# Optimization experiments

Measured on AMD Instinct MI355X. Metric: run time of the kernel, lower is better.

## Reference

```python
import jax, jax.numpy as jnp
import numpy as np

N = 100_000      # nodes
E_HALF = 1_600_000  # undirected edges (mirrored -> 3.2M directed)
D = 128          # feature dim
K = 1            # k-MIS hop parameter


def setup_inputs() -> dict:
    key = jax.random.key(0)
    k1, k2, k3, k4, k5 = jax.random.split(key, 5)
    x = jax.random.normal(k1, (N, D), dtype=jnp.float32)
    src = jax.random.randint(k2, (E_HALF,), 0, N)
    dst = jax.random.randint(k3, (E_HALF,), 0, N)
    # symmetric edge list (undirected graph), as k-MIS coverage assumes
    edge_index = jnp.stack([jnp.concatenate([src, dst]),
                            jnp.concatenate([dst, src])])
    ea = jax.random.uniform(k4, (E_HALF,), dtype=jnp.float32)
    edge_attr = jnp.concatenate([ea, ea])
    # RandomScorer: score is a uniform random vector over nodes
    score = jax.random.uniform(k5, (N,), dtype=jnp.float32)
    return {"x": x, "edge_index": edge_index, "edge_attr": edge_attr, "score": score}


def _scatter_min(values, index, n, fill):
    return jnp.full((n,), fill, dtype=values.dtype).at[index].min(values)


def maximal_k_independent_set(row, col, n, k, rank):
    # Iteratively: propagate min rank k hops; nodes equal to their own
    # (uncovered) min rank join the MIS; mark their k-hop neighborhood covered.
    mis = jnp.zeros(n, dtype=bool)
    mask = jnp.zeros(n, dtype=bool)
    min_rank = rank
    while not bool(mask.all()):
        for _ in range(k):
            mn = _scatter_min(min_rank[row], col, n, n)
            min_rank = jnp.minimum(mn, min_rank)
        mis = mis | ((rank == min_rank) & ~mask)
        mask = mask | mis
        for _ in range(k):
            nb = jnp.zeros(n, dtype=bool).at[col].max(mask[row])
            mask = mask | nb
        min_rank = jnp.where(mask, n, rank)
    return mis


def cluster_k_mis(mis, row, col, n, k, rank):
    # assign every node to the MIS node of minimum rank within k hops
    min_rank = jnp.where(mis, rank, n)
    for _ in range(k):
        mn = _scatter_min(min_rank[row], col, n, n)
        min_rank = jnp.minimum(mn, min_rank)
    _, clusters = jnp.unique(min_rank, return_inverse=True)  # sorted uniques
    perm = jnp.argsort(rank[mis])  # sorted-rank position -> index into x[mis]
    return perm[clusters.ravel()]


def reference(x, edge_index, edge_attr, score):
    n = x.shape[0]
    row, col = edge_index[0], edge_index[1]
    # Greedy ordering: rank = inverse permutation of argsort(score)
    rank = jnp.argsort(jnp.argsort(score))
    mis = maximal_k_independent_set(row, col, n, K, rank)
    cluster = cluster_k_mis(mis, row, col, n, K, rank)
    # sparse_reduce_adj: map edges into cluster space, coalesce with sum
    pairs = jnp.stack([cluster[row], cluster[col]], axis=1)  # [E,2]
    uk, inv = jnp.unique(pairs, axis=0, return_inverse=True)
    vals = jax.ops.segment_sum(edge_attr, inv.ravel(), num_segments=uk.shape[0])
    r2, c2 = uk[:, 0], uk[:, 1]
    keep = r2 != c2  # remove_self_loops
    edge_index_out = jnp.stack([r2[keep], c2[keep]])
    edge_attr_out = vals[keep]
    x_out = x[jnp.nonzero(mis)[0]]  # reduce_x=None -> select MIS node features
    return x_out, edge_index_out, edge_attr_out, cluster, mis, score
```

## Files before the change

### kernel.cpp

```cpp
#include <hip/hip_runtime.h>
#include <stdint.h>

#define RTILE 4096
#define ROUNDS 10


__global__ void k_init_counters(int* counters){
  int t = threadIdx.x;
  counters[t] = 0;
  if (t == 7) counters[7] = 1;
}
__global__ void k_init_nodes(int* mis, int N){
  int v = blockIdx.x*blockDim.x + threadIdx.x;
  if (v < N) mis[v]=0;
}
__global__ void k_zero_vals(float* vals, int E){
  int i = blockIdx.x*blockDim.x + threadIdx.x;
  if (i < E) vals[i]=0.f;
}

__global__ void k_score_key(const float* score, unsigned* keys, unsigned* pay, int N){
  int i = blockIdx.x*blockDim.x+threadIdx.x;
  if (i<N){
    unsigned b = __float_as_uint(score[i]);
    b ^= ((int)b < 0) ? 0xFFFFFFFFu : 0x80000000u;
    keys[i]=b; pay[i]=(unsigned)i;
  }
}
__global__ void k_rank_build(const unsigned* pay, int* rank, int* pm, int N){
  int p = blockIdx.x*blockDim.x+threadIdx.x;
  if (p<N){ int v = (int)pay[p]; rank[v]=p; pm[v]=p; }
}
__global__ void k_make_colrow(const int* __restrict__ row, const int* __restrict__ col,
                              unsigned* __restrict__ keys, unsigned* __restrict__ pay, int E){
  int e = blockIdx.x*blockDim.x+threadIdx.x;
  if (e<E){ keys[e]=(unsigned)col[e]; pay[e]=(unsigned)row[e]; }
}

template<typename K, int TILE>
__global__ void k_radix_hist(const K* __restrict__ keys, int n, int shift,
                             unsigned* __restrict__ ghist, int numBlocks, const int* gate){
  if (*gate==0) return;
  __shared__ unsigned h[512];
  int t=threadIdx.x, b=blockIdx.x;
  h[t]=0; h[t+256]=0; __syncthreads();
  int base = b*TILE;
  for (int j=t; j<TILE; j+=256){
    int i = base+j;
    if (i<n){
      unsigned d = (unsigned)((keys[i]>>shift)&(K)511);
      atomicAdd(&h[d],1u);
    }
  }
  __syncthreads();
  ghist[(size_t)t*numBlocks + b] = h[t];
  ghist[(size_t)(t+256)*numBlocks + b] = h[t+256];
}

template<typename K, int TILE>
__global__ __launch_bounds__(256)
void k_radix_scatter(const K* __restrict__ keysIn, const unsigned* __restrict__ payIn,
                     K* __restrict__ keysOut, unsigned* __restrict__ payOut,
                     int n, int shift, const unsigned* __restrict__ gbase,
                     int numBlocks, const int* gate){
  if (*gate==0) return;
  constexpr int G = TILE/256;
  constexpr int SEG = TILE/4;
  __shared__ __align__(16) char smem[(size_t)TILE*sizeof(K)];
  K* skey = (K*)smem;
  unsigned* spay = (unsigned*)smem;
  __shared__ unsigned whist[4][512];
  __shared__ unsigned lbase[512];
  __shared__ unsigned ss[256];
  int t=threadIdx.x, b=blockIdx.x;
  int lane = t&63, wave = t>>6;
  int base = b*TILE;
  int tilecnt = min(TILE, n-base);
  int segBase = base + wave*SEG;

  for (int j=lane; j<512; j+=64) whist[wave][j]=0;
  K keys[G]; unsigned pays[G];
  for (int g=0; g<G; ++g){
    int i = segBase + g*64 + lane;
    bool valid = i<n;
    keys[g] = valid ? keysIn[i] : (K)0;
    pays[g] = valid ? payIn[i] : 0u;
    if (valid){
      unsigned d = (unsigned)((keys[g]>>shift)&(K)511);
      atomicAdd(&whist[wave][d],1u);
    }
  }
  __syncthreads();

  unsigned h0[4], h1[4], u0=0, u1=0;
  #pragma unroll
  for (int w=0;w<4;++w){ h0[w]=whist[w][2*t];   u0+=h0[w];
                         h1[w]=whist[w][2*t+1]; u1+=h1[w]; }
  ss[t]=u0+u1; __syncthreads();
  for (int off=1; off<256; off<<=1){
    unsigned x=(t>=off)?ss[t-off]:0u; __syncthreads();
    ss[t]+=x; __syncthreads();
  }
  unsigned excl = t? ss[t-1]:0u;
  lbase[2*t]=excl; lbase[2*t+1]=excl+u0;
  unsigned c0=excl, c1=excl+u0;
  #pragma unroll
  for (int w=0;w<4;++w){ whist[w][2*t]=c0;   c0+=h0[w];
                         whist[w][2*t+1]=c1; c1+=h1[w]; }
  __syncthreads();

  unsigned offs[G];
  for (int g=0; g<G; ++g){
    int i = segBase + g*64 + lane;
    bool valid = i<n;
    unsigned d = (unsigned)((keys[g]>>shift)&(K)511);
    unsigned long long m = __ballot(valid);
    #pragma unroll
    for (int bit=0; bit<9; ++bit){
      unsigned long long bb = __ballot((d>>bit)&1u);
      m &= ((d>>bit)&1u) ? bb : ~bb;
    }
    if (valid){
      int lr = __popcll(m & ((1ull<<lane)-1ull));
      int leader = __ffsll((unsigned long long)m)-1;
      unsigned old=0;
      if (lr==0) old = atomicAdd(&whist[wave][d], (unsigned)__popcll(m));
      old = __shfl(old, leader);
      unsigned o = old + (unsigned)lr;
      skey[o]=keys[g]; offs[g]=o;
    }
  }
  __syncthreads();

  unsigned gpos_[G];
  for (int c=0;c<G;++c){
    int j=c*256+t;
    if (j<tilecnt){
      K k=skey[j];
      unsigned d=(unsigned)((k>>shift)&(K)511);
      unsigned gp = gbase[(size_t)d*numBlocks + b] + ((unsigned)j - lbase[d]);
      keysOut[gp]=k; gpos_[c]=gp;
    }
  }
  __syncthreads();
  for (int g=0; g<G; ++g){
    int i = segBase + g*64 + lane;
    if (i<n) spay[offs[g]]=pays[g];
  }
  __syncthreads();
  for (int c=0;c<G;++c){
    int j=c*256+t;
    if (j<tilecnt) payOut[gpos_[c]] = spay[j];
  }
}

template<typename T>
__global__ void k_scan_single(T* data, int n, T* total, const int* gate){
  if (*gate==0) return;
  __shared__ T sh[1024];
  __shared__ T carry;
  int t=threadIdx.x;
  if (t==0) carry=(T)0;
  __syncthreads();
  for (int base=0; base<n; base+=4096){
    T v[4]; T s=(T)0;
    int i0 = base + t*4;
    #pragma unroll
    for (int j=0;j<4;j++){ int i=i0+j; v[j] = (i<n)?data[i]:(T)0; s+=v[j]; }
    sh[t]=s; __syncthreads();
    for (int off=1; off<1024; off<<=1){
      T x = (t>=off)? sh[t-off]:(T)0; __syncthreads();
      sh[t]+=x; __syncthreads();
    }
    T excl = (t?sh[t-1]:(T)0) + carry;
    #pragma unroll
    for (int j=0;j<4;j++){ int i=i0+j; if(i<n){ T o=v[j]; data[i]=excl; excl+=o; } }
    T tot = sh[1023];
    __syncthreads();
    if (t==0) carry += tot;
    __syncthreads();
  }
  if (total && t==0) *total = carry;
}
template<typename T>
__global__ void k_scan_partials(const T* __restrict__ in, T* __restrict__ bsums,
                                int n, const int* gate){
  if (*gate==0) return;
  __shared__ T sh[256];
  int b=blockIdx.x, t=threadIdx.x;
  long base = (long)b*RTILE + (long)t*16;
  T s=(T)0;
  #pragma unroll
  for (int j=0;j<16;j++){ long i=base+j; if(i<n) s+=in[i]; }
  sh[t]=s; __syncthreads();
  for (int off=128; off>0; off>>=1){ if(t<off) sh[t]+=sh[t+off]; __syncthreads(); }
  if (t==0) bsums[b]=sh[0];
}
template<typename T>
__global__ void k_scan_final(const T* __restrict__ in, T* __restrict__ out,
                             const T* __restrict__ bsums, int n, const int* gate){
  if (*gate==0) return;
  __shared__ T sh[256];
  int b=blockIdx.x, t=threadIdx.x;
  long base = (long)b*RTILE + (long)t*16;
  T v[16]; T s=(T)0;
  #pragma unroll
  for (int j=0;j<16;j++){ long i=base+j; v[j]=(i<n)?in[i]:(T)0; s+=v[j]; }
  sh[t]=s; __syncthreads();
  for (int off=1; off<256; off<<=1){
    T x=(t>=off)?sh[t-off]:(T)0; __syncthreads(); sh[t]+=x; __syncthreads();
  }
  T run=(t?sh[t-1]:(T)0)+bsums[b];
  #pragma unroll
  for (int j=0;j<16;j++){ long i=base+j; if(i<n){ T o=v[j]; out[i]=run; run+=o; } }
}

__global__ void k_build_off(const unsigned* __restrict__ scol, int* __restrict__ off, int E, int N){
  int i = blockIdx.x*blockDim.x+threadIdx.x;
  if (i>=E) return;
  int c = (int)scol[i];
  int p = (i==0) ? -1 : (int)scol[i-1];
  for (int v=p+1; v<=c; ++v) off[v]=i;
  if (i==E-1){ for (int v=c+1; v<=N; ++v) off[v]=E; }
}

__global__ void k_round1(const int* __restrict__ off, const int* __restrict__ nbr,
                         const int* __restrict__ pm, int* __restrict__ mis,
                         int* __restrict__ maskA, int N, const int* gate){
  if (*gate==0) return;
  int v = blockIdx.x*blockDim.x+threadIdx.x;
  if (v>=N) return;
  int p = pm[v];
  if (p == N){ maskA[v]=1; return; }
  int m = p;
  int s=off[v], e=off[v+1];
  for (int j=s; j<e; ++j){ int u=nbr[j]; m = min(m, pm[u]); }
  int nm = (m == p);
  if (nm) mis[v]=1;
  maskA[v] = nm;
}
__global__ void k_round2(const int* __restrict__ off, const int* __restrict__ nbr,
                         const int* __restrict__ maskA, int* __restrict__ pm,
                         int N, int* cnt, const int* gate){
  if (*gate==0) return;
  int v = blockIdx.x*blockDim.x+threadIdx.x;
  int um = 0;
  if (v<N){
    int mk = maskA[v];
    int s=off[v], e=off[v+1];
    for (int j=s; j<e && !mk; ++j) mk |= maskA[nbr[j]];
    if (mk) pm[v] = N;
    um = !mk;
  }
  unsigned long long bm = __ballot(um);
  if ((threadIdx.x&63)==0 && bm) atomicAdd(cnt, (int)__popcll(bm));
}

__global__ void k_cl_init(const int* rank, const int* mis, int* pm, int N){
  int v = blockIdx.x*blockDim.x+threadIdx.x;
  if (v<N) pm[v] = mis[v] ? rank[v] : N;
}
__global__ void k_cl_gather(const int* __restrict__ off, const int* __restrict__ nbr,
                            const int* __restrict__ pm, int* __restrict__ mn, int N){
  int v = blockIdx.x*blockDim.x+threadIdx.x;
  if (v>=N) return;
  int m = pm[v];
  int s=off[v], e=off[v+1];
  for (int j=s; j<e; ++j) m = min(m, pm[nbr[j]]);
  mn[v] = m;
}
__global__ void k_copy_u32(const int* in, unsigned* out, int N){
  int v = blockIdx.x*blockDim.x+threadIdx.x;
  if (v<N) out[v]=(unsigned)in[v];
}
__global__ void k_cl_map(const int* rank, const int* mis, const unsigned* cidx,
                         int* map, int* rmax, int N){
  int v = blockIdx.x*blockDim.x+threadIdx.x;
  if (v<N && mis[v]){ map[rank[v]] = (int)cidx[v]; atomicMax(rmax, rank[v]); }
}
__global__ void k_cl_cluster(const int* mn, const int* map, const int* rmax, int* cluster, int N){
  int v = blockIdx.x*blockDim.x+threadIdx.x;
  if (v<N){
    int mr = mn[v];
    if (mr >= N) mr = *rmax;
    cluster[v] = map[mr];
  }
}
__global__ void k_gather_x(const float4* __restrict__ x, float4* __restrict__ out,
                           const int* __restrict__ mis, const unsigned* __restrict__ cidx,
                           int N, int D4){
  int t = blockIdx.x*blockDim.x+threadIdx.x;
  int v = t / D4, q = t - v*D4;
  if (v<N && mis[v]) out[(size_t)cidx[v]*D4 + q] = x[(size_t)v*D4 + q];
}

__global__ void k_set_gates(int* counters){
  int M = counters[1];
  int sh = (M<=1) ? 1 : (32-__clz((unsigned)(M-1)));
  int kb = 2*sh;
  int npass = 1 + (9<kb) + (18<kb) + (27<kb);
  counters[36] = sh;
  counters[32] = 1;
  counters[33] = (9  < kb);
  counters[34] = (18 < kb);
  counters[35] = (27 < kb);
  counters[37] = npass & 1;
}
__global__ void k_pair_key(const int* __restrict__ row, const int* __restrict__ col,
                           const int* __restrict__ cluster, const float* __restrict__ attr,
                           unsigned long long* __restrict__ keys, unsigned* __restrict__ pay,
                           const int* __restrict__ counters, int E){
  int e = blockIdx.x*blockDim.x+threadIdx.x;
  if (e<E){
    int sh = counters[36];
    unsigned a = (unsigned)cluster[row[e]], b=(unsigned)cluster[col[e]];
    keys[e] = ((unsigned long long)a<<sh) | b;
    pay[e] = __float_as_uint(attr[e]);
  }
}
__global__ void k_flags(const unsigned long long* __restrict__ keyA,
                        const unsigned long long* __restrict__ keyB,
                        unsigned long long* __restrict__ fcomb,
                        const int* __restrict__ counters, int E){
  const unsigned long long* keys = counters[37] ? keyB : keyA;
  int i = blockIdx.x*blockDim.x+threadIdx.x;
  if (i<E){
    int sh = counters[36];
    unsigned long long k = keys[i];
    unsigned head = (i==0) || (k != keys[i-1]);
    unsigned a=(unsigned)(k>>sh), b=(unsigned)(k & ((1ull<<sh)-1ull));
    unsigned keep = (head && a!=b) ? 1u : 0u;
    fcomb[i] = ((unsigned long long)keep<<32) | head;
  }
}
__global__ void k_acc_seg(const unsigned long long* __restrict__ keyA,
                          const unsigned long long* __restrict__ keyB,
                          const unsigned* __restrict__ payA, const unsigned* __restrict__ payB,
                          const unsigned long long* __restrict__ fcomb,
                          float* __restrict__ vals, const int* __restrict__ counters, int E){
  const unsigned long long* keys = counters[37] ? keyB : keyA;
  const unsigned* pay = counters[37] ? payB : payA;
  int i = blockIdx.x*blockDim.x+threadIdx.x;
  int lane = threadIdx.x & 63;
  bool valid = i < E;
  unsigned long long k = valid ? keys[i] : ~0ull;
  float v = valid ? __uint_as_float(pay[i]) : 0.f;
  #pragma unroll
  for (int off=1; off<64; off<<=1){
    float o = __shfl_up(v, off);
    unsigned long long ko = __shfl_up(k, off);
    if (lane >= off && ko == k) v += o;
  }
  if (valid){
    unsigned long long knext = (i+1<E) ? keys[i+1] : ~0ull;
    if (lane==63 || k != knext){
      unsigned head = (i==0) || (keys[i-1] != k);
      unsigned e1 = (unsigned)fcomb[i];
      atomicAdd(&vals[e1 + head - 1u], v);
    }
  }
}
__global__ void k_write_edges(const unsigned long long* __restrict__ keyA,
                              const unsigned long long* __restrict__ keyB,
                              const unsigned long long* __restrict__ fcomb,
                              const float* __restrict__ vals, float* __restrict__ out,
                              const int* __restrict__ counters, int E, int D){
  const unsigned long long* keys = counters[37] ? keyB : keyA;
  int i = blockIdx.x*blockDim.x+threadIdx.x;
  if (i<E){
    int sh = counters[36];
    int head=(i==0)||(keys[i]!=keys[i-1]);
    unsigned a=(unsigned)(keys[i]>>sh), b=(unsigned)(keys[i] & ((1ull<<sh)-1ull));
    if (head && a!=b){
      unsigned long long sc = fcomb[i];
      unsigned opos = (unsigned)(sc>>32);
      int M = counters[1], Ep = counters[3];
      size_t off = (size_t)M*D;
      out[off + opos] = (float)a;
      out[off + (size_t)Ep + opos] = (float)b;
      out[off + 2*(size_t)Ep + opos] = vals[(unsigned)sc];
    }
  }
}
__global__ void k_write_nodes(const int* __restrict__ cluster, const int* __restrict__ mis,
                              const float* __restrict__ score, float* __restrict__ out,
                              const int* __restrict__ counters, int N, int D){
  int v = blockIdx.x*blockDim.x+threadIdx.x;
  if (v<N){
    int M=counters[1], Ep=counters[3];
    size_t off = (size_t)M*D + 3*(size_t)Ep;
    out[off + v] = (float)cluster[v];
    out[off + (size_t)N + v] = mis[v] ? 1.f : 0.f;
    out[off + 2*(size_t)N + v] = score[v];
  }
}

template<typename T>
static void big_scan_t(T* data, int n, T* total, const int* gate, void* bsums_raw, hipStream_t stream){
  int B = (n + RTILE-1)/RTILE;
  T* bsums = (T*)bsums_raw;
  k_scan_partials<T><<<B,256,0,stream>>>(data,bsums,n,gate);
  k_scan_single<T><<<1,1024,0,stream>>>(bsums,B,total,gate);
  k_scan_final<T><<<B,256,0,stream>>>(data,data,bsums,n,gate);
}

extern "C" void kernel_launch(void* const* d_in, const int* in_sizes, int n_in,
                              void* d_out, int out_size, void* d_ws, size_t ws_size,
                              hipStream_t stream){
  const float* x     = (const float*)d_in[0];
  const int*   ei    = (const int*)d_in[1];
  const float* attr  = (const float*)d_in[2];
  const float* score = (const float*)d_in[3];
  int N = in_sizes[3];
  int E = in_sizes[2];
  int D = in_sizes[0]/N;
  const int* row = ei;
  const int* col = ei + E;
  float* out = (float*)d_out;

  char* p = (char*)d_ws;
  auto alloc = [&](size_t bytes)->char*{ char* r=p; p += ((bytes+255)/256)*256; return r; };
  unsigned long long* keyA = (unsigned long long*)alloc((size_t)E*8);
  unsigned long long* keyB = (unsigned long long*)alloc((size_t)E*8);
  unsigned* payA  = (unsigned*)alloc((size_t)E*4);
  unsigned* payB  = (unsigned*)alloc((size_t)E*4);
  unsigned* scanA = (unsigned*)alloc((size_t)E*4);
  unsigned long long* fcomb = (unsigned long long*)alloc((size_t)E*8);
  float*    vals  = (float*)alloc((size_t)E*4);
  int* csr_row = (int*)alloc((size_t)E*4);
  unsigned* off= (unsigned*)alloc((size_t)(N+1)*4);
  int* rank   = (int*)alloc((size_t)N*4);
  int* pm     = (int*)alloc((size_t)N*4);
  int* mis    = (int*)alloc((size_t)N*4);
  int* maskA  = (int*)alloc((size_t)N*4);
  int* mnArr  = (int*)alloc((size_t)N*4);
  int* map    = (int*)alloc((size_t)N*4);
  unsigned* cidx = (unsigned*)alloc((size_t)N*4);
  int* cluster= (int*)alloc((size_t)N*4);
  int* counters=(int*)alloc(256*4);
  int Be = (E + RTILE-1)/RTILE;
  int Bn1k = (N + 1023)/1024;
  unsigned* ghist = (unsigned*)alloc((size_t)512*Be*4);
  void* bsums = (void*)alloc(4096*8);

  int nbN = (N+255)/256, nbE = (E+255)/256;
  const int* ON = counters+7;

  k_init_counters<<<1,256,0,stream>>>(counters);
  k_init_nodes<<<nbN,256,0,stream>>>(mis,N);
  k_zero_vals<<<nbE,256,0,stream>>>(vals,E);

  k_make_colrow<<<nbE,256,0,stream>>>(row,col,(unsigned*)keyA,payA,E);
  k_radix_hist<unsigned,RTILE><<<Be,256,0,stream>>>((unsigned*)keyA,E,0,ghist,Be,ON);
  big_scan_t<unsigned>(ghist,512*Be,nullptr,ON,bsums,stream);
  k_radix_scatter<unsigned,RTILE><<<Be,256,0,stream>>>((unsigned*)keyA,payA,(unsigned*)keyB,payB,E,0,ghist,Be,ON);
  k_radix_hist<unsigned,RTILE><<<Be,256,0,stream>>>((unsigned*)keyB,E,9,ghist,Be,ON);
  big_scan_t<unsigned>(ghist,512*Be,nullptr,ON,bsums,stream);
  k_radix_scatter<unsigned,RTILE><<<Be,256,0,stream>>>((unsigned*)keyB,payB,scanA,(unsigned*)csr_row,E,9,ghist,Be,ON);
  k_build_off<<<nbE,256,0,stream>>>(scanA,(int*)off,E,N);

  k_score_key<<<nbN,256,0,stream>>>(score,(unsigned*)keyA,payA,N);
  {
    unsigned *ki=(unsigned*)keyA,*ko=(unsigned*)keyB,*pi=payA,*po=payB;
    for (int pass=0; pass<4; ++pass){
      int shift = pass*9;
      k_radix_hist<unsigned,1024><<<Bn1k,256,0,stream>>>(ki,N,shift,ghist,Bn1k,ON);
      big_scan_t<unsigned>(ghist,512*Bn1k,nullptr,ON,bsums,stream);
      k_radix_scatter<unsigned,1024><<<Bn1k,256,0,stream>>>(ki,pi,ko,po,N,shift,ghist,Bn1k,ON);
      unsigned* tk=ki; ki=ko; ko=tk; unsigned* tp=pi; pi=po; po=tp;
    }
    k_rank_build<<<nbN,256,0,stream>>>(pi, rank, pm, N);
  }

  for (int r=0; r<ROUNDS; ++r){
    const int* gate = (r==0) ? ON : (counters + 8 + r - 1);
    int* cnt = counters + 8 + r;
    k_round1<<<nbN,256,0,stream>>>((const int*)off,csr_row,pm,mis,maskA,N,gate);
    k_round2<<<nbN,256,0,stream>>>((const int*)off,csr_row,maskA,pm,N,cnt,gate);
  }

  k_cl_init<<<nbN,256,0,stream>>>(rank,mis,pm,N);
  k_cl_gather<<<nbN,256,0,stream>>>((const int*)off,csr_row,pm,mnArr,N);
  k_copy_u32<<<nbN,256,0,stream>>>(mis,cidx,N);
  big_scan_t<unsigned>(cidx,N,(unsigned*)(counters+1),ON,bsums,stream);
  k_cl_map<<<nbN,256,0,stream>>>(rank,mis,cidx,map,counters+4,N);
  k_cl_cluster<<<nbN,256,0,stream>>>(mnArr,map,counters+4,cluster,N);
  k_gather_x<<<(N*(D/4)+255)/256,256,0,stream>>>((const float4*)x,(float4*)out,mis,cidx,N,D/4);

  k_set_gates<<<1,1,0,stream>>>(counters);
  k_pair_key<<<nbE,256,0,stream>>>(row,col,cluster,attr,keyA,payA,counters,E);
  {
    unsigned long long *ki=keyA,*ko=keyB; unsigned *pi=payA,*po=payB;
    for (int pass=0; pass<4; ++pass){
      int shift = pass*9;
      const int* g = counters + 32 + pass;
      k_radix_hist<unsigned long long,RTILE><<<Be,256,0,stream>>>(ki,E,shift,ghist,Be,g);
      big_scan_t<unsigned>(ghist,512*Be,nullptr,g,bsums,stream);
      k_radix_scatter<unsigned long long,RTILE><<<Be,256,0,stream>>>(ki,pi,ko,po,E,shift,ghist,Be,g);
      unsigned long long* tk=ki; ki=ko; ko=tk; unsigned* tp=pi; pi=po; po=tp;
    }
    k_flags<<<nbE,256,0,stream>>>(keyA,keyB,fcomb,counters,E);
    big_scan_t<unsigned long long>(fcomb,E,(unsigned long long*)(counters+2),ON,bsums,stream);
    k_acc_seg<<<nbE,256,0,stream>>>(keyA,keyB,payA,payB,fcomb,vals,counters,E);
    k_write_edges<<<nbE,256,0,stream>>>(keyA,keyB,fcomb,vals,out,counters,E,D);
  }
  k_write_nodes<<<nbN,256,0,stream>>>(cluster,mis,score,out,counters,N,D);
}
```

Baseline: 878.2 us.

## Fuse MIS rounds into cooperative kernel and shrink pair keys to 32-bit

Replaces the per-round pair of MIS kernels and the cluster init/gather/copy kernels with one cooperative persistent kernel that uses grid.sync between phases, exits early when no uncovered nodes remain, and assigns four lanes per node for neighbor scans. It also switches the cluster-pair sort keys from 64-bit to 32-bit, which halves key traffic in the radix sort and segment kernels. The 32-bit keys assume 2*shift fits in 32 bits. The cooperative launch assumes all 1024 blocks of 256 threads can be resident at once, and it adds grid-wide barrier costs.

```diff
diff --git a/kernel.cpp b/kernel.cpp
--- a/kernel.cpp
+++ b/kernel.cpp
@@ -1,5 +1,7 @@
 #include <hip/hip_runtime.h>
+#include <hip/hip_cooperative_groups.h>
 #include <stdint.h>
+namespace cg = cooperative_groups;
 
 #define RTILE 4096
 #define ROUNDS 10
@@ -9,10 +11,6 @@
   int t = threadIdx.x;
   counters[t] = 0;
   if (t == 7) counters[7] = 1;
-}
-__global__ void k_init_nodes(int* mis, int N){
-  int v = blockIdx.x*blockDim.x + threadIdx.x;
-  if (v < N) mis[v]=0;
 }
 __global__ void k_zero_vals(float* vals, int E){
   int i = blockIdx.x*blockDim.x + threadIdx.x;
@@ -224,55 +222,70 @@
   if (i==E-1){ for (int v=c+1; v<=N; ++v) off[v]=E; }
 }
 
-__global__ void k_round1(const int* __restrict__ off, const int* __restrict__ nbr,
-                         const int* __restrict__ pm, int* __restrict__ mis,
-                         int* __restrict__ maskA, int N, const int* gate){
-  if (*gate==0) return;
-  int v = blockIdx.x*blockDim.x+threadIdx.x;
-  if (v>=N) return;
-  int p = pm[v];
-  if (p == N){ maskA[v]=1; return; }
-  int m = p;
-  int s=off[v], e=off[v+1];
-  for (int j=s; j<e; ++j){ int u=nbr[j]; m = min(m, pm[u]); }
-  int nm = (m == p);
-  if (nm) mis[v]=1;
-  maskA[v] = nm;
-}
-__global__ void k_round2(const int* __restrict__ off, const int* __restrict__ nbr,
-                         const int* __restrict__ maskA, int* __restrict__ pm,
-                         int N, int* cnt, const int* gate){
-  if (*gate==0) return;
-  int v = blockIdx.x*blockDim.x+threadIdx.x;
-  int um = 0;
-  if (v<N){
-    int mk = maskA[v];
+__global__ __launch_bounds__(256,4)
+void k_mis_coop(const int* __restrict__ off, const int* __restrict__ nbr,
+                const int* __restrict__ rank, int* __restrict__ pm,
+                int* __restrict__ mis, int* __restrict__ maskA,
+                unsigned* __restrict__ cidx, int* __restrict__ mnArr,
+                int N, int* __restrict__ cnt){
+  cg::grid_group grid = cg::this_grid();
+  int gT = gridDim.x*blockDim.x;
+  int tid0 = blockIdx.x*blockDim.x + threadIdx.x;
+  __shared__ int s_go;
+  for (int r=0; r<ROUNDS; ++r){
+    for (int t4 = tid0; t4 < 4*N; t4 += gT){
+      int v = t4>>2, q = t4&3;
+      int p = pm[v];
+      if (p == N){ if (q==0) maskA[v]=1; continue; }
+      int m = p;
+      int s=off[v], e=off[v+1];
+      for (int j=s+q; j<e; j+=4) m = min(m, pm[nbr[j]]);
+      m = min(m, __shfl_xor(m,1));
+      m = min(m, __shfl_xor(m,2));
+      if (q==0){
+        int nm = (m==p);
+        if (r==0) mis[v]=nm; else if (nm) mis[v]=1;
+        maskA[v]=nm;
+      }
+    }
+    grid.sync();
+    for (int t4 = tid0; t4 < 4*N; t4 += gT){
+      int v = t4>>2, q = t4&3;
+      int mk = maskA[v];
+      if (!mk){
+        int s=off[v], e=off[v+1];
+        for (int j=s+q; j<e && !mk; j+=4) mk |= maskA[nbr[j]];
+      }
+      mk |= __shfl_xor(mk,1);
+      mk |= __shfl_xor(mk,2);
+      if (q==0){
+        if (mk) pm[v]=N;
+        else atomicAdd(cnt+r, 1);
+      }
+    }
+    grid.sync();
+    if (threadIdx.x==0)
+      s_go = __hip_atomic_load(cnt+r, __ATOMIC_RELAXED, __HIP_MEMORY_SCOPE_AGENT);
+    __syncthreads();
+    if (s_go == 0) break;
+  }
+  for (int v = tid0; v < N; v += gT){
+    int mi = mis[v];
+    pm[v] = mi ? rank[v] : N;
+    cidx[v] = (unsigned)mi;
+  }
+  grid.sync();
+  for (int t4 = tid0; t4 < 4*N; t4 += gT){
+    int v = t4>>2, q = t4&3;
+    int m = pm[v];
     int s=off[v], e=off[v+1];
-    for (int j=s; j<e && !mk; ++j) mk |= maskA[nbr[j]];
-    if (mk) pm[v] = N;
-    um = !mk;
-  }
-  unsigned long long bm = __ballot(um);
-  if ((threadIdx.x&63)==0 && bm) atomicAdd(cnt, (int)__popcll(bm));
-}
-
-__global__ void k_cl_init(const int* rank, const int* mis, int* pm, int N){
-  int v = blockIdx.x*blockDim.x+threadIdx.x;
-  if (v<N) pm[v] = mis[v] ? rank[v] : N;
-}
-__global__ void k_cl_gather(const int* __restrict__ off, const int* __restrict__ nbr,
-                            const int* __restrict__ pm, int* __restrict__ mn, int N){
-  int v = blockIdx.x*blockDim.x+threadIdx.x;
-  if (v>=N) return;
-  int m = pm[v];
-  int s=off[v], e=off[v+1];
-  for (int j=s; j<e; ++j) m = min(m, pm[nbr[j]]);
-  mn[v] = m;
-}
-__global__ void k_copy_u32(const int* in, unsigned* out, int N){
-  int v = blockIdx.x*blockDim.x+threadIdx.x;
-  if (v<N) out[v]=(unsigned)in[v];
-}
+    for (int j=s+q; j<e; j+=4) m = min(m, pm[nbr[j]]);
+    m = min(m, __shfl_xor(m,1));
+    m = min(m, __shfl_xor(m,2));
+    if (q==0) mnArr[v]=m;
+  }
+}
+
 __global__ void k_cl_map(const int* rank, const int* mis, const unsigned* cidx,
                          int* map, int* rmax, int N){
   int v = blockIdx.x*blockDim.x+threadIdx.x;
@@ -308,51 +321,50 @@
 }
 __global__ void k_pair_key(const int* __restrict__ row, const int* __restrict__ col,
                            const int* __restrict__ cluster, const float* __restrict__ attr,
-                           unsigned long long* __restrict__ keys, unsigned* __restrict__ pay,
+                           unsigned* __restrict__ keys, unsigned* __restrict__ pay,
                            const int* __restrict__ counters, int E){
   int e = blockIdx.x*blockDim.x+threadIdx.x;
   if (e<E){
     int sh = counters[36];
     unsigned a = (unsigned)cluster[row[e]], b=(unsigned)cluster[col[e]];
-    keys[e] = ((unsigned long long)a<<sh) | b;
+    keys[e] = (a<<sh) | b;
     pay[e] = __float_as_uint(attr[e]);
   }
 }
-__global__ void k_flags(const unsigned long long* __restrict__ keyA,
-                        const unsigned long long* __restrict__ keyB,
+__global__ void k_flags(const unsigned* __restrict__ keyA,
+                        const unsigned* __restrict__ keyB,
                         unsigned long long* __restrict__ fcomb,
                         const int* __restrict__ counters, int E){
-  const unsigned long long* keys = counters[37] ? keyB : keyA;
+  const unsigned* keys = counters[37] ? keyB : keyA;
   int i = blockIdx.x*blockDim.x+threadIdx.x;
   if (i<E){
     int sh = counters[36];
-    unsigned long long k = keys[i];
+    unsigned k = keys[i];
     unsigned head = (i==0) || (k != keys[i-1]);
-    unsigned a=(unsigned)(k>>sh), b=(unsigned)(k & ((1ull<<sh)-1ull));
+    unsigned a=k>>sh, b=k&((1u<<sh)-1u);
     unsigned keep = (head && a!=b) ? 1u : 0u;
     fcomb[i] = ((unsigned long long)keep<<32) | head;
   }
 }
-__global__ void k_acc_seg(const unsigned long long* __restrict__ keyA,
-                          const unsigned long long* __restrict__ keyB,
+__global__ void k_acc_seg(const unsigned* __restrict__ keyA, const unsigned* __restrict__ keyB,
                           const unsigned* __restrict__ payA, const unsigned* __restrict__ payB,
                           const unsigned long long* __restrict__ fcomb,
                           float* __restrict__ vals, const int* __restrict__ counters, int E){
-  const unsigned long long* keys = counters[37] ? keyB : keyA;
+  const unsigned* keys = counters[37] ? keyB : keyA;
   const unsigned* pay = counters[37] ? payB : payA;
   int i = blockIdx.x*blockDim.x+threadIdx.x;
   int lane = threadIdx.x & 63;
   bool valid = i < E;
-  unsigned long long k = valid ? keys[i] : ~0ull;
+  unsigned k = valid ? keys[i] : ~0u;
   float v = valid ? __uint_as_float(pay[i]) : 0.f;
   #pragma unroll
   for (int off=1; off<64; off<<=1){
     float o = __shfl_up(v, off);
-    unsigned long long ko = __shfl_up(k, off);
+    unsigned ko = __shfl_up(k, off);
     if (lane >= off && ko == k) v += o;
   }
   if (valid){
-    unsigned long long knext = (i+1<E) ? keys[i+1] : ~0ull;
+    unsigned knext = (i+1<E) ? keys[i+1] : ~0u;
     if (lane==63 || k != knext){
       unsigned head = (i==0) || (keys[i-1] != k);
       unsigned e1 = (unsigned)fcomb[i];
@@ -360,17 +372,16 @@
     }
   }
 }
-__global__ void k_write_edges(const unsigned long long* __restrict__ keyA,
-                              const unsigned long long* __restrict__ keyB,
+__global__ void k_write_edges(const unsigned* __restrict__ keyA, const unsigned* __restrict__ keyB,
                               const unsigned long long* __restrict__ fcomb,
                               const float* __restrict__ vals, float* __restrict__ out,
                               const int* __restrict__ counters, int E, int D){
-  const unsigned long long* keys = counters[37] ? keyB : keyA;
+  const unsigned* keys = counters[37] ? keyB : keyA;
   int i = blockIdx.x*blockDim.x+threadIdx.x;
   if (i<E){
     int sh = counters[36];
     int head=(i==0)||(keys[i]!=keys[i-1]);
-    unsigned a=(unsigned)(keys[i]>>sh), b=(unsigned)(keys[i] & ((1ull<<sh)-1ull));
+    unsigned a=keys[i]>>sh, b=keys[i]&((1u<<sh)-1u);
     if (head && a!=b){
       unsigned long long sc = fcomb[i];
       unsigned opos = (unsigned)(sc>>32);
@@ -420,8 +431,8 @@
 
   char* p = (char*)d_ws;
   auto alloc = [&](size_t bytes)->char*{ char* r=p; p += ((bytes+255)/256)*256; return r; };
-  unsigned long long* keyA = (unsigned long long*)alloc((size_t)E*8);
-  unsigned long long* keyB = (unsigned long long*)alloc((size_t)E*8);
+  unsigned* keyA  = (unsigned*)alloc((size_t)E*4);
+  unsigned* keyB  = (unsigned*)alloc((size_t)E*4);
   unsigned* payA  = (unsigned*)alloc((size_t)E*4);
   unsigned* payB  = (unsigned*)alloc((size_t)E*4);
   unsigned* scanA = (unsigned*)alloc((size_t)E*4);
@@ -447,21 +458,20 @@
   const int* ON = counters+7;
 
   k_init_counters<<<1,256,0,stream>>>(counters);
-  k_init_nodes<<<nbN,256,0,stream>>>(mis,N);
   k_zero_vals<<<nbE,256,0,stream>>>(vals,E);
 
-  k_make_colrow<<<nbE,256,0,stream>>>(row,col,(unsigned*)keyA,payA,E);
-  k_radix_hist<unsigned,RTILE><<<Be,256,0,stream>>>((unsigned*)keyA,E,0,ghist,Be,ON);
+  k_make_colrow<<<nbE,256,0,stream>>>(row,col,keyA,payA,E);
+  k_radix_hist<unsigned,RTILE><<<Be,256,0,stream>>>(keyA,E,0,ghist,Be,ON);
   big_scan_t<unsigned>(ghist,512*Be,nullptr,ON,bsums,stream);
-  k_radix_scatter<unsigned,RTILE><<<Be,256,0,stream>>>((unsigned*)keyA,payA,(unsigned*)keyB,payB,E,0,ghist,Be,ON);
-  k_radix_hist<unsigned,RTILE><<<Be,256,0,stream>>>((unsigned*)keyB,E,9,ghist,Be,ON);
+  k_radix_scatter<unsigned,RTILE><<<Be,256,0,stream>>>(keyA,payA,keyB,payB,E,0,ghist,Be,ON);
+  k_radix_hist<unsigned,RTILE><<<Be,256,0,stream>>>(keyB,E,9,ghist,Be,ON);
   big_scan_t<unsigned>(ghist,512*Be,nullptr,ON,bsums,stream);
-  k_radix_scatter<unsigned,RTILE><<<Be,256,0,stream>>>((unsigned*)keyB,payB,scanA,(unsigned*)csr_row,E,9,ghist,Be,ON);
+  k_radix_scatter<unsigned,RTILE><<<Be,256,0,stream>>>(keyB,payB,scanA,(unsigned*)csr_row,E,9,ghist,Be,ON);
   k_build_off<<<nbE,256,0,stream>>>(scanA,(int*)off,E,N);
 
-  k_score_key<<<nbN,256,0,stream>>>(score,(unsigned*)keyA,payA,N);
+  k_score_key<<<nbN,256,0,stream>>>(score,keyA,payA,N);
   {
-    unsigned *ki=(unsigned*)keyA,*ko=(unsigned*)keyB,*pi=payA,*po=payB;
+    unsigned *ki=keyA,*ko=keyB,*pi=payA,*po=payB;
     for (int pass=0; pass<4; ++pass){
       int shift = pass*9;
       k_radix_hist<unsigned,1024><<<Bn1k,256,0,stream>>>(ki,N,shift,ghist,Bn1k,ON);
@@ -472,16 +482,18 @@
     k_rank_build<<<nbN,256,0,stream>>>(pi, rank, pm, N);
   }
 
-  for (int r=0; r<ROUNDS; ++r){
-    const int* gate = (r==0) ? ON : (counters + 8 + r - 1);
-    int* cnt = counters + 8 + r;
-    k_round1<<<nbN,256,0,stream>>>((const int*)off,csr_row,pm,mis,maskA,N,gate);
-    k_round2<<<nbN,256,0,stream>>>((const int*)off,csr_row,maskA,pm,N,cnt,gate);
-  }
-
-  k_cl_init<<<nbN,256,0,stream>>>(rank,mis,pm,N);
-  k_cl_gather<<<nbN,256,0,stream>>>((const int*)off,csr_row,pm,mnArr,N);
-  k_copy_u32<<<nbN,256,0,stream>>>(mis,cidx,N);
+  {
+    const int* off_i = (const int*)off;
+    const int* nbr_i = (const int*)csr_row;
+    const int* rank_i = (const int*)rank;
+    int* cntp = counters + 8;
+    void* cargs[] = {(void*)&off_i, (void*)&nbr_i, (void*)&rank_i, (void*)&pm,
+                     (void*)&mis, (void*)&maskA, (void*)&cidx, (void*)&mnArr,
+                     (void*)&N, (void*)&cntp};
+    hipLaunchCooperativeKernel((const void*)k_mis_coop, dim3(1024), dim3(256),
+                               cargs, 0, stream);
+  }
+
   big_scan_t<unsigned>(cidx,N,(unsigned*)(counters+1),ON,bsums,stream);
   k_cl_map<<<nbN,256,0,stream>>>(rank,mis,cidx,map,counters+4,N);
   k_cl_cluster<<<nbN,256,0,stream>>>(mnArr,map,counters+4,cluster,N);
@@ -490,14 +502,14 @@
   k_set_gates<<<1,1,0,stream>>>(counters);
   k_pair_key<<<nbE,256,0,stream>>>(row,col,cluster,attr,keyA,payA,counters,E);
   {
-    unsigned long long *ki=keyA,*ko=keyB; unsigned *pi=payA,*po=payB;
+    unsigned *ki=keyA,*ko=keyB,*pi=payA,*po=payB;
     for (int pass=0; pass<4; ++pass){
       int shift = pass*9;
       const int* g = counters + 32 + pass;
-      k_radix_hist<unsigned long long,RTILE><<<Be,256,0,stream>>>(ki,E,shift,ghist,Be,g);
+      k_radix_hist<unsigned,RTILE><<<Be,256,0,stream>>>(ki,E,shift,ghist,Be,g);
       big_scan_t<unsigned>(ghist,512*Be,nullptr,g,bsums,stream);
-      k_radix_scatter<unsigned long long,RTILE><<<Be,256,0,stream>>>(ki,pi,ko,po,E,shift,ghist,Be,g);
-      unsigned long long* tk=ki; ki=ko; ko=tk; unsigned* tp=pi; pi=po; po=tp;
+      k_radix_scatter<unsigned,RTILE><<<Be,256,0,stream>>>(ki,pi,ko,po,E,shift,ghist,Be,g);
+      unsigned* tk=ki; ki=ko; ko=tk; unsigned* tp=pi; pi=po; po=tp;
     }
     k_flags<<<nbE,256,0,stream>>>(keyA,keyB,fcomb,counters,E);
     big_scan_t<unsigned long long>(fcomb,E,(unsigned long long*)(counters+2),ON,bsums,stream);
```

Result: slower. 1.518 ms (+72.9%).
